# Performance work log

Hardware: AMD Instinct MI355X
Metric: run time of the kernel (lower is better)

## Reference

```python
import jax, jax.numpy as jnp
import numpy as np

K = 11            # involution kernel size
GC = 16           # involution group channels
EPS = 1e-5        # BatchNorm eps


def bn(x, g, b, m, v):
    # eval-mode BatchNorm2d with running stats
    inv = g / jnp.sqrt(v + EPS)
    return x * inv[None, :, None, None] + (b - m * inv)[None, :, None, None]


def conv1x1(x, w, b=None):
    y = jnp.einsum('bchw,oc->bohw', x, w)
    if b is not None:
        y = y + b[None, :, None, None]
    return y


def setup_inputs() -> dict:
    key = jax.random.key(0)
    ks = jax.random.split(key, 32)
    C = 128          # inplanes == planes
    Cm = C // 2      # 64, involution channels
    Mid = Cm // 4    # 16, involution reduce channels
    G = Cm // GC     # 4 groups
    SE = C // 16     # 8
    B, H, W = 1, 160, 160
    f32 = jnp.float32
    rn = lambda k, shape, s=0.05: (jax.random.normal(k, shape, dtype=f32) * s)
    pv = lambda k, n: jax.random.uniform(k, (n,), dtype=f32, minval=0.5, maxval=1.5)
    return {
        'x': jax.random.normal(ks[0], (B, C, H, W), dtype=f32),
        'g1': pv(ks[1], C), 'b1': rn(ks[2], (C,)), 'm1': rn(ks[3], (C,), 0.1), 'v1': pv(ks[4], C),
        'w1': rn(ks[5], (Cm, C)),
        'g2': pv(ks[6], Cm), 'b2': rn(ks[7], (Cm,)), 'm2': rn(ks[8], (Cm,), 0.1), 'v2': pv(ks[9], Cm),
        'inv_w1': rn(ks[10], (Mid, Cm)),
        'ig': pv(ks[11], Mid), 'ib': rn(ks[12], (Mid,)), 'im': rn(ks[13], (Mid,), 0.1), 'iv': pv(ks[14], Mid),
        'inv_w2': rn(ks[15], (K * K * G, Mid)), 'inv_b2': rn(ks[16], (K * K * G,)),
        'g3': pv(ks[17], Cm), 'b3': rn(ks[18], (Cm,)), 'm3': rn(ks[19], (Cm,), 0.1), 'v3': pv(ks[20], Cm),
        'w3': rn(ks[21], (C, Cm)),
        'se_w1': rn(ks[22], (SE, C)), 'se_b1': rn(ks[23], (SE,)),
        'se_w2': rn(ks[24], (C, SE)), 'se_b2': rn(ks[25], (C,)),
    }


def reference(x, g1, b1, m1, v1, w1, g2, b2, m2, v2,
              inv_w1, ig, ib, im, iv, inv_w2, inv_b2,
              g3, b3, m3, v3, w3, se_w1, se_b1, se_w2, se_b2):
    identity = x
    out = jax.nn.elu(bn(x, g1, b1, m1, v1))
    out = conv1x1(out, w1)                              # (B, Cm, H, W)
    out = jax.nn.elu(bn(out, g2, b2, m2, v2))

    # ----- involution(channels=Cm, kernel=11, stride=1) -----
    B, Cm, H, W = out.shape
    G = Cm // GC
    t = jax.nn.relu(bn(conv1x1(out, inv_w1), ig, ib, im, iv))
    wk = conv1x1(t, inv_w2, inv_b2)                     # (B, G*K*K, H, W)
    wk = wk.reshape(B, G, K * K, H, W)
    p = K // 2
    # patches channel order: [C, kh, kw] -> matches torch unfold
    patches = jax.lax.conv_general_dilated_patches(
        out, (K, K), (1, 1), ((p, p), (p, p)))         # (B, Cm*K*K, H, W)
    patches = patches.reshape(B, G, GC, K * K, H, W)
    out = jnp.einsum('bgkhw,bgckhw->bgchw', wk, patches).reshape(B, Cm, H, W)
    # ---------------------------------------------------------

    out = jax.nn.elu(bn(out, g3, b3, m3, v3))
    out = conv1x1(out, w3)                              # (B, C, H, W)

    # SE module
    s = out.mean(axis=(2, 3), keepdims=True)            # (B, C, 1, 1)
    s = jax.nn.relu(conv1x1(s, se_w1, se_b1))
    s = jax.nn.sigmoid(conv1x1(s, se_w2, se_b2))
    return out * s + identity
```

## Files before the change

### kernel.cpp

```cpp
#include <hip/hip_runtime.h>
#include <math.h>

#define HPIX 160
#define WPIX 160
#define NPIX 25600
#define C0   128
#define CM   64
#define MID  16
#define KK   11
#define KK2  121
#define PAD  5
#define PADW 176
#define PADH 170
#define CHP  (PADH*PADW)
#define NBX  (NPIX/256)
#define BN_EPS 1e-5f

__device__ __forceinline__ float elu_f(float y) { return y > 0.f ? y : expm1f(y); }

__global__ __launch_bounds__(256) void k_act(
        const float* __restrict__ x,
        const float* __restrict__ g1, const float* __restrict__ b1,
        const float* __restrict__ m1, const float* __restrict__ v1,
        float* __restrict__ act) {
    int i4 = blockIdx.x * 256 + threadIdx.x;
    int c = i4 / (NPIX / 4);
    float inv  = g1[c] * rsqrtf(v1[c] + BN_EPS);
    float beta = b1[c] - m1[c] * inv;
    float4 xv = ((const float4*)x)[i4];
    float4 o;
    o.x = elu_f(fmaf(xv.x, inv, beta));
    o.y = elu_f(fmaf(xv.y, inv, beta));
    o.z = elu_f(fmaf(xv.z, inv, beta));
    o.w = elu_f(fmaf(xv.w, inv, beta));
    ((float4*)act)[i4] = o;
}

__global__ __launch_bounds__(256, 4) void k_conv1(
        const float* __restrict__ act, const float* __restrict__ w1,
        const float* __restrict__ g2, const float* __restrict__ b2,
        const float* __restrict__ m2, const float* __restrict__ v2,
        float* __restrict__ feat_pad) {
    const int tid = threadIdx.x;
    const int p   = blockIdx.x * 256 + tid;
    const int oc0 = blockIdx.y * 16;
    const float* wbase = w1 + oc0 * C0;

    float acc[16] = {0,0,0,0,0,0,0,0,0,0,0,0,0,0,0,0};
    #pragma unroll 4
    for (int k = 0; k < C0; ++k) {
        float a = act[k * NPIX + p];
        #pragma unroll
        for (int j = 0; j < 16; ++j)
            acc[j] = fmaf(wbase[j * C0 + k], a, acc[j]);
    }

    const int h = p / WPIX, w = p % WPIX;
    const int off = (h + PAD) * PADW + (w + PAD);
    #pragma unroll
    for (int j = 0; j < 16; ++j) {
        int c = oc0 + j;
        float inv = g2[c] * rsqrtf(v2[c] + BN_EPS);
        float y = acc[j] * inv + (b2[c] - m2[c] * inv);
        feat_pad[c * CHP + off] = elu_f(y);
    }
}

__global__ __launch_bounds__(256, 4) void k_conv_t(
        const float* __restrict__ feat_pad, const float* __restrict__ wt,
        const float* __restrict__ g, const float* __restrict__ b,
        const float* __restrict__ m, const float* __restrict__ v,
        float* __restrict__ t) {
    const int tid = threadIdx.x;
    const int p   = blockIdx.x * 256 + tid;
    const int oc0 = blockIdx.y * 4;
    const int h = p / WPIX, w = p % WPIX;
    const int off = (h + PAD) * PADW + (w + PAD);

    float acc[4] = {0,0,0,0};
    #pragma unroll 8
    for (int k = 0; k < CM; ++k) {
        float a = feat_pad[k * CHP + off];
        #pragma unroll
        for (int j = 0; j < 4; ++j)
            acc[j] = fmaf(wt[(oc0 + j) * CM + k], a, acc[j]);
    }
    #pragma unroll
    for (int j = 0; j < 4; ++j) {
        int c = oc0 + j;
        float inv = g[c] * rsqrtf(v[c] + BN_EPS);
        t[c * NPIX + p] = fmaxf(acc[j] * inv + (b[c] - m[c] * inv), 0.f);
    }
}

__global__ __launch_bounds__(256, 4) void k_involution(
        const float* __restrict__ t, const float* __restrict__ feat_pad,
        const float* __restrict__ inv_w2, const float* __restrict__ inv_b2,
        const float* __restrict__ g3, const float* __restrict__ b3,
        const float* __restrict__ m3, const float* __restrict__ v3,
        float* __restrict__ out) {
    __shared__ float s_wk[484 * 16];
    __shared__ float s_t[MID * 16];

    const int q   = gridDim.x >> 3;
    const int b   = blockIdx.x;
    const int bid = (b & 7) * q + (b >> 3);

    const int tid = threadIdx.x;
    const int p0  = bid * 16;
    const int px  = tid & 15;
    const int c4  = tid >> 4;

    s_t[tid] = t[c4 * NPIX + p0 + px];
    __syncthreads();

    {
        float tr[MID];
        #pragma unroll
        for (int mm = 0; mm < MID; ++mm) tr[mm] = s_t[mm * 16 + px];
        for (int j = c4; j < 484; j += 16) {
            const float4* wrow = (const float4*)(inv_w2 + j * MID);
            float acc = inv_b2[j];
            #pragma unroll
            for (int qq = 0; qq < 4; ++qq) {
                float4 wv = wrow[qq];
                acc = fmaf(wv.x, tr[qq*4+0], acc);
                acc = fmaf(wv.y, tr[qq*4+1], acc);
                acc = fmaf(wv.z, tr[qq*4+2], acc);
                acc = fmaf(wv.w, tr[qq*4+3], acc);
            }
            s_wk[j * 16 + px] = acc;
        }
    }
    __syncthreads();

    const int tx = tid & 3;
    const int c  = tid >> 2;
    const int g  = c >> 4;
    const int h  = p0 / WPIX;
    const int wb = (p0 % WPIX) + tx * 4;
    const float* fbase = feat_pad + c * CHP + h * PADW + wb;
    const float* wkb   = s_wk + (g * KK2) * 16 + tx * 4;

    float acc0 = 0.f, acc1 = 0.f, acc2 = 0.f, acc3 = 0.f;
    #pragma unroll 2
    for (int kh = 0; kh < KK; ++kh) {
        const float4* fp = (const float4*)(fbase + kh * PADW);
        float4 A = fp[0], B = fp[1], Cq = fp[2], D = fp[3];
        float f[16] = {A.x,A.y,A.z,A.w, B.x,B.y,B.z,B.w,
                       Cq.x,Cq.y,Cq.z,Cq.w, D.x,D.y,D.z,D.w};
        const float* wr = wkb + kh * KK * 16;
        #pragma unroll
        for (int kw = 0; kw < KK; ++kw) {
            float4 wv = *(const float4*)(wr + kw * 16);
            acc0 = fmaf(wv.x, f[kw + 0], acc0);
            acc1 = fmaf(wv.y, f[kw + 1], acc1);
            acc2 = fmaf(wv.z, f[kw + 2], acc2);
            acc3 = fmaf(wv.w, f[kw + 3], acc3);
        }
    }

    float inv  = g3[c] * rsqrtf(v3[c] + BN_EPS);
    float beta = b3[c] - m3[c] * inv;
    float4 o;
    o.x = elu_f(fmaf(acc0, inv, beta));
    o.y = elu_f(fmaf(acc1, inv, beta));
    o.z = elu_f(fmaf(acc2, inv, beta));
    o.w = elu_f(fmaf(acc3, inv, beta));
    *(float4*)(out + c * NPIX + p0 + tx * 4) = o;
}

__global__ __launch_bounds__(256, 4) void k_conv3(
        const float* __restrict__ in, const float* __restrict__ w,
        float* __restrict__ out, float* __restrict__ parts) {
    const int tid = threadIdx.x;
    const int p   = blockIdx.x * 256 + tid;
    const int oc0 = blockIdx.y * 16;
    const float* wbase = w + oc0 * CM;

    float acc[16] = {0,0,0,0,0,0,0,0,0,0,0,0,0,0,0,0};
    #pragma unroll 4
    for (int k = 0; k < CM; ++k) {
        float a = in[k * NPIX + p];
        #pragma unroll
        for (int j = 0; j < 16; ++j)
            acc[j] = fmaf(wbase[j * CM + k], a, acc[j]);
    }
    #pragma unroll
    for (int j = 0; j < 16; ++j)
        out[(oc0 + j) * NPIX + p] = acc[j];

    __shared__ float s_red[16][4];
    const int lane = tid & 63, wid = tid >> 6;
    #pragma unroll
    for (int j = 0; j < 16; ++j) {
        float s = acc[j];
        #pragma unroll
        for (int off = 32; off; off >>= 1) s += __shfl_down(s, off);
        if (lane == 0) s_red[j][wid] = s;
    }
    __syncthreads();
    if (tid < 16) {
        float s = s_red[tid][0] + s_red[tid][1] + s_red[tid][2] + s_red[tid][3];
        parts[(oc0 + tid) * NBX + blockIdx.x] = s;
    }
}

__global__ void k_se(const float* __restrict__ parts,
                     const float* __restrict__ w1, const float* __restrict__ b1,
                     const float* __restrict__ w2, const float* __restrict__ b2,
                     float* __restrict__ scale) {
    __shared__ float s_p[C0];
    __shared__ float s_h[8];
    int tid = threadIdx.x;
    float s = 0.f;
    for (int i = 0; i < NBX; ++i) s += parts[tid * NBX + i];
    s_p[tid] = s * (1.f / NPIX);
    __syncthreads();
    if (tid < 8) {
        float acc = b1[tid];
        for (int c = 0; c < C0; ++c) acc = fmaf(w1[tid * C0 + c], s_p[c], acc);
        s_h[tid] = fmaxf(acc, 0.f);
    }
    __syncthreads();
    float acc = b2[tid];
    #pragma unroll
    for (int j = 0; j < 8; ++j) acc = fmaf(w2[tid * 8 + j], s_h[j], acc);
    scale[tid] = 1.f / (1.f + expf(-acc));
}

__global__ __launch_bounds__(256) void k_final(
        const float* __restrict__ pre, const float* __restrict__ scale,
        const float* __restrict__ x, float* __restrict__ out) {
    int i4 = blockIdx.x * 256 + threadIdx.x;
    int c = i4 / (NPIX / 4);
    float sc = scale[c];
    float4 pv = ((const float4*)pre)[i4];
    float4 xv = ((const float4*)x)[i4];
    float4 o;
    o.x = fmaf(pv.x, sc, xv.x);
    o.y = fmaf(pv.y, sc, xv.y);
    o.z = fmaf(pv.z, sc, xv.z);
    o.w = fmaf(pv.w, sc, xv.w);
    ((float4*)out)[i4] = o;
}

extern "C" void kernel_launch(void* const* d_in, const int* in_sizes, int n_in,
                              void* d_out, int out_size, void* d_ws, size_t ws_size,
                              hipStream_t stream) {
    const float* x      = (const float*)d_in[0];
    const float* g1     = (const float*)d_in[1];
    const float* b1     = (const float*)d_in[2];
    const float* m1     = (const float*)d_in[3];
    const float* v1     = (const float*)d_in[4];
    const float* w1     = (const float*)d_in[5];
    const float* g2     = (const float*)d_in[6];
    const float* b2     = (const float*)d_in[7];
    const float* m2     = (const float*)d_in[8];
    const float* v2     = (const float*)d_in[9];
    const float* inv_w1 = (const float*)d_in[10];
    const float* ig     = (const float*)d_in[11];
    const float* ib     = (const float*)d_in[12];
    const float* im     = (const float*)d_in[13];
    const float* iv     = (const float*)d_in[14];
    const float* inv_w2 = (const float*)d_in[15];
    const float* inv_b2 = (const float*)d_in[16];
    const float* g3     = (const float*)d_in[17];
    const float* b3     = (const float*)d_in[18];
    const float* m3     = (const float*)d_in[19];
    const float* v3     = (const float*)d_in[20];
    const float* w3     = (const float*)d_in[21];
    const float* se_w1  = (const float*)d_in[22];
    const float* se_b1  = (const float*)d_in[23];
    const float* se_w2  = (const float*)d_in[24];
    const float* se_b2  = (const float*)d_in[25];
    float* out = (float*)d_out;

    float* ws       = (float*)d_ws;
    float* act      = ws;
    float* feat_pad = act + C0 * NPIX;
    float* buf_t    = feat_pad + CM * CHP;
    float* buf5     = act;
    float* buf6     = buf_t + MID * NPIX;
    float* parts    = feat_pad;
    float* scale    = buf6 + C0 * NPIX;

    hipMemsetAsync(feat_pad, 0, (size_t)CM * CHP * sizeof(float), stream);

    k_act<<<(C0 * NPIX / 4) / 256, 256, 0, stream>>>(x, g1, b1, m1, v1, act);

    k_conv1<<<dim3(NBX, CM / 16), 256, 0, stream>>>(
        act, w1, g2, b2, m2, v2, feat_pad);

    k_conv_t<<<dim3(NBX, MID / 4), 256, 0, stream>>>(
        feat_pad, inv_w1, ig, ib, im, iv, buf_t);

    k_involution<<<NPIX / 16, 256, 0, stream>>>(buf_t, feat_pad, inv_w2, inv_b2,
                                                g3, b3, m3, v3, buf5);

    k_conv3<<<dim3(NBX, C0 / 16), 256, 0, stream>>>(buf5, w3, buf6, parts);

    k_se<<<1, C0, 0, stream>>>(parts, se_w1, se_b1, se_w2, se_b2, scale);

    k_final<<<(C0 * NPIX / 4) / 256, 256, 0, stream>>>(buf6, scale, x, out);
}
```

Baseline: 123.9 us.

## Halve involution block size with two channels per thread; vectorize conv weight loads

The involution kernel now runs 128 threads per block, and each thread computes two channels. This lets the same shared-memory kernel weights serve two channels' feature loads, and the dynamic-kernel generation step computes two rows per iteration with split accumulators. The 1x1 conv kernels (conv1, conv_t, conv3) now load four input channels at a time and read weights as float4 instead of scalars. The aim is fewer instructions per FMA and more reuse, at the cost of higher register pressure and fewer threads per block in the involution kernel.

Measured after the change: 148.0 us. 1.19x slower.

```diff
diff --git a/kernel.cpp b/kernel.cpp
--- a/kernel.cpp
+++ b/kernel.cpp
@@ -47,12 +47,20 @@
     const float* wbase = w1 + oc0 * C0;
 
     float acc[16] = {0,0,0,0,0,0,0,0,0,0,0,0,0,0,0,0};
-    #pragma unroll 4
-    for (int k = 0; k < C0; ++k) {
-        float a = act[k * NPIX + p];
-        #pragma unroll
-        for (int j = 0; j < 16; ++j)
-            acc[j] = fmaf(wbase[j * C0 + k], a, acc[j]);
+    #pragma unroll 2
+    for (int k0 = 0; k0 < C0; k0 += 4) {
+        float a0 = act[(k0 + 0) * NPIX + p];
+        float a1 = act[(k0 + 1) * NPIX + p];
+        float a2 = act[(k0 + 2) * NPIX + p];
+        float a3 = act[(k0 + 3) * NPIX + p];
+        #pragma unroll
+        for (int j = 0; j < 16; ++j) {
+            float4 wv = *(const float4*)(wbase + j * C0 + k0);
+            acc[j] = fmaf(wv.x, a0, acc[j]);
+            acc[j] = fmaf(wv.y, a1, acc[j]);
+            acc[j] = fmaf(wv.z, a2, acc[j]);
+            acc[j] = fmaf(wv.w, a3, acc[j]);
+        }
     }
 
     const int h = p / WPIX, w = p % WPIX;
@@ -78,12 +86,20 @@
     const int off = (h + PAD) * PADW + (w + PAD);
 
     float acc[4] = {0,0,0,0};
-    #pragma unroll 8
-    for (int k = 0; k < CM; ++k) {
-        float a = feat_pad[k * CHP + off];
-        #pragma unroll
-        for (int j = 0; j < 4; ++j)
-            acc[j] = fmaf(wt[(oc0 + j) * CM + k], a, acc[j]);
+    #pragma unroll 4
+    for (int k0 = 0; k0 < CM; k0 += 4) {
+        float a0 = feat_pad[(k0 + 0) * CHP + off];
+        float a1 = feat_pad[(k0 + 1) * CHP + off];
+        float a2 = feat_pad[(k0 + 2) * CHP + off];
+        float a3 = feat_pad[(k0 + 3) * CHP + off];
+        #pragma unroll
+        for (int j = 0; j < 4; ++j) {
+            float4 wv = *(const float4*)(wt + (oc0 + j) * CM + k0);
+            acc[j] = fmaf(wv.x, a0, acc[j]);
+            acc[j] = fmaf(wv.y, a1, acc[j]);
+            acc[j] = fmaf(wv.z, a2, acc[j]);
+            acc[j] = fmaf(wv.w, a3, acc[j]);
+        }
     }
     #pragma unroll
     for (int j = 0; j < 4; ++j) {
@@ -93,7 +109,7 @@
     }
 }
 
-__global__ __launch_bounds__(256, 4) void k_involution(
+__global__ __launch_bounds__(128, 4) void k_involution(
         const float* __restrict__ t, const float* __restrict__ feat_pad,
         const float* __restrict__ inv_w2, const float* __restrict__ inv_b2,
         const float* __restrict__ g3, const float* __restrict__ b3,
@@ -109,65 +125,124 @@
     const int tid = threadIdx.x;
     const int p0  = bid * 16;
     const int px  = tid & 15;
-    const int c4  = tid >> 4;
-
-    s_t[tid] = t[c4 * NPIX + p0 + px];
+
+    s_t[tid]       = t[(tid >> 4) * NPIX + p0 + (tid & 15)];
+    s_t[tid + 128] = t[((tid >> 4) + 8) * NPIX + p0 + (tid & 15)];
     __syncthreads();
 
     {
-        float tr[MID];
-        #pragma unroll
-        for (int mm = 0; mm < MID; ++mm) tr[mm] = s_t[mm * 16 + px];
-        for (int j = c4; j < 484; j += 16) {
-            const float4* wrow = (const float4*)(inv_w2 + j * MID);
-            float acc = inv_b2[j];
-            #pragma unroll
-            for (int qq = 0; qq < 4; ++qq) {
-                float4 wv = wrow[qq];
-                acc = fmaf(wv.x, tr[qq*4+0], acc);
-                acc = fmaf(wv.y, tr[qq*4+1], acc);
-                acc = fmaf(wv.z, tr[qq*4+2], acc);
-                acc = fmaf(wv.w, tr[qq*4+3], acc);
-            }
-            s_wk[j * 16 + px] = acc;
+        float tr0  = s_t[0*16+px],  tr1  = s_t[1*16+px];
+        float tr2  = s_t[2*16+px],  tr3  = s_t[3*16+px];
+        float tr4  = s_t[4*16+px],  tr5  = s_t[5*16+px];
+        float tr6  = s_t[6*16+px],  tr7  = s_t[7*16+px];
+        float tr8  = s_t[8*16+px],  tr9  = s_t[9*16+px];
+        float tr10 = s_t[10*16+px], tr11 = s_t[11*16+px];
+        float tr12 = s_t[12*16+px], tr13 = s_t[13*16+px];
+        float tr14 = s_t[14*16+px], tr15 = s_t[15*16+px];
+        const int jb = tid >> 4;
+
+        for (int j = jb; j + 8 < 484; j += 16) {
+            const float4* wa = (const float4*)(inv_w2 + j * MID);
+            const float4* wc = (const float4*)(inv_w2 + (j + 8) * MID);
+            float4 a0 = wa[0], a1 = wa[1], a2 = wa[2], a3 = wa[3];
+            float4 c0 = wc[0], c1 = wc[1], c2 = wc[2], c3 = wc[3];
+            float aL = inv_b2[j],     aH = 0.f;
+            float cL = inv_b2[j + 8], cH = 0.f;
+            aL = fmaf(a0.x, tr0, aL);  aL = fmaf(a0.y, tr1, aL);
+            aL = fmaf(a0.z, tr2, aL);  aL = fmaf(a0.w, tr3, aL);
+            aL = fmaf(a1.x, tr4, aL);  aL = fmaf(a1.y, tr5, aL);
+            aL = fmaf(a1.z, tr6, aL);  aL = fmaf(a1.w, tr7, aL);
+            aH = fmaf(a2.x, tr8, aH);  aH = fmaf(a2.y, tr9, aH);
+            aH = fmaf(a2.z, tr10, aH); aH = fmaf(a2.w, tr11, aH);
+            aH = fmaf(a3.x, tr12, aH); aH = fmaf(a3.y, tr13, aH);
+            aH = fmaf(a3.z, tr14, aH); aH = fmaf(a3.w, tr15, aH);
+            cL = fmaf(c0.x, tr0, cL);  cL = fmaf(c0.y, tr1, cL);
+            cL = fmaf(c0.z, tr2, cL);  cL = fmaf(c0.w, tr3, cL);
+            cL = fmaf(c1.x, tr4, cL);  cL = fmaf(c1.y, tr5, cL);
+            cL = fmaf(c1.z, tr6, cL);  cL = fmaf(c1.w, tr7, cL);
+            cH = fmaf(c2.x, tr8, cH);  cH = fmaf(c2.y, tr9, cH);
+            cH = fmaf(c2.z, tr10, cH); cH = fmaf(c2.w, tr11, cH);
+            cH = fmaf(c3.x, tr12, cH); cH = fmaf(c3.y, tr13, cH);
+            cH = fmaf(c3.z, tr14, cH); cH = fmaf(c3.w, tr15, cH);
+            s_wk[j * 16 + px]       = aL + aH;
+            s_wk[(j + 8) * 16 + px] = cL + cH;
+        }
+        if (jb < 4) {
+            int j = 480 + jb;
+            const float4* wa = (const float4*)(inv_w2 + j * MID);
+            float4 a0 = wa[0], a1 = wa[1], a2 = wa[2], a3 = wa[3];
+            float aL = inv_b2[j], aH = 0.f;
+            aL = fmaf(a0.x, tr0, aL);  aL = fmaf(a0.y, tr1, aL);
+            aL = fmaf(a0.z, tr2, aL);  aL = fmaf(a0.w, tr3, aL);
+            aL = fmaf(a1.x, tr4, aL);  aL = fmaf(a1.y, tr5, aL);
+            aL = fmaf(a1.z, tr6, aL);  aL = fmaf(a1.w, tr7, aL);
+            aH = fmaf(a2.x, tr8, aH);  aH = fmaf(a2.y, tr9, aH);
+            aH = fmaf(a2.z, tr10, aH); aH = fmaf(a2.w, tr11, aH);
+            aH = fmaf(a3.x, tr12, aH); aH = fmaf(a3.y, tr13, aH);
+            aH = fmaf(a3.z, tr14, aH); aH = fmaf(a3.w, tr15, aH);
+            s_wk[j * 16 + px] = aL + aH;
         }
     }
     __syncthreads();
 
     const int tx = tid & 3;
-    const int c  = tid >> 2;
-    const int g  = c >> 4;
+    const int cp = tid >> 2;
+    const int c0 = cp * 2;
+    const int g  = c0 >> 4;
     const int h  = p0 / WPIX;
     const int wb = (p0 % WPIX) + tx * 4;
-    const float* fbase = feat_pad + c * CHP + h * PADW + wb;
-    const float* wkb   = s_wk + (g * KK2) * 16 + tx * 4;
-
-    float acc0 = 0.f, acc1 = 0.f, acc2 = 0.f, acc3 = 0.f;
+    const float* f0b = feat_pad + c0 * CHP + h * PADW + wb;
+    const float* f1b = f0b + CHP;
+    const float* wkb = s_wk + (g * KK2) * 16 + tx * 4;
+
+    float a00 = 0.f, a01 = 0.f, a02 = 0.f, a03 = 0.f;
+    float a10 = 0.f, a11 = 0.f, a12 = 0.f, a13 = 0.f;
     #pragma unroll 2
     for (int kh = 0; kh < KK; ++kh) {
-        const float4* fp = (const float4*)(fbase + kh * PADW);
-        float4 A = fp[0], B = fp[1], Cq = fp[2], D = fp[3];
-        float f[16] = {A.x,A.y,A.z,A.w, B.x,B.y,B.z,B.w,
-                       Cq.x,Cq.y,Cq.z,Cq.w, D.x,D.y,D.z,D.w};
+        const float4* p0f = (const float4*)(f0b + kh * PADW);
+        float4 A0 = p0f[0], B0 = p0f[1], Cq0 = p0f[2], D0 = p0f[3];
+        const float4* p1f = (const float4*)(f1b + kh * PADW);
+        float4 A1 = p1f[0], B1 = p1f[1], Cq1 = p1f[2], D1 = p1f[3];
+        float f0[16] = {A0.x,A0.y,A0.z,A0.w, B0.x,B0.y,B0.z,B0.w,
+                        Cq0.x,Cq0.y,Cq0.z,Cq0.w, D0.x,D0.y,D0.z,D0.w};
+        float f1[16] = {A1.x,A1.y,A1.z,A1.w, B1.x,B1.y,B1.z,B1.w,
+                        Cq1.x,Cq1.y,Cq1.z,Cq1.w, D1.x,D1.y,D1.z,D1.w};
         const float* wr = wkb + kh * KK * 16;
         #pragma unroll
         for (int kw = 0; kw < KK; ++kw) {
             float4 wv = *(const float4*)(wr + kw * 16);
-            acc0 = fmaf(wv.x, f[kw + 0], acc0);
-            acc1 = fmaf(wv.y, f[kw + 1], acc1);
-            acc2 = fmaf(wv.z, f[kw + 2], acc2);
-            acc3 = fmaf(wv.w, f[kw + 3], acc3);
-        }
-    }
-
-    float inv  = g3[c] * rsqrtf(v3[c] + BN_EPS);
-    float beta = b3[c] - m3[c] * inv;
-    float4 o;
-    o.x = elu_f(fmaf(acc0, inv, beta));
-    o.y = elu_f(fmaf(acc1, inv, beta));
-    o.z = elu_f(fmaf(acc2, inv, beta));
-    o.w = elu_f(fmaf(acc3, inv, beta));
-    *(float4*)(out + c * NPIX + p0 + tx * 4) = o;
+            a00 = fmaf(wv.x, f0[kw + 0], a00);
+            a01 = fmaf(wv.y, f0[kw + 1], a01);
+            a02 = fmaf(wv.z, f0[kw + 2], a02);
+            a03 = fmaf(wv.w, f0[kw + 3], a03);
+            a10 = fmaf(wv.x, f1[kw + 0], a10);
+            a11 = fmaf(wv.y, f1[kw + 1], a11);
+            a12 = fmaf(wv.z, f1[kw + 2], a12);
+            a13 = fmaf(wv.w, f1[kw + 3], a13);
+        }
+    }
+
+    {
+        float inv  = g3[c0] * rsqrtf(v3[c0] + BN_EPS);
+        float beta = b3[c0] - m3[c0] * inv;
+        float4 o;
+        o.x = elu_f(fmaf(a00, inv, beta));
+        o.y = elu_f(fmaf(a01, inv, beta));
+        o.z = elu_f(fmaf(a02, inv, beta));
+        o.w = elu_f(fmaf(a03, inv, beta));
+        *(float4*)(out + c0 * NPIX + p0 + tx * 4) = o;
+    }
+    {
+        int c1 = c0 + 1;
+        float inv  = g3[c1] * rsqrtf(v3[c1] + BN_EPS);
+        float beta = b3[c1] - m3[c1] * inv;
+        float4 o;
+        o.x = elu_f(fmaf(a10, inv, beta));
+        o.y = elu_f(fmaf(a11, inv, beta));
+        o.z = elu_f(fmaf(a12, inv, beta));
+        o.w = elu_f(fmaf(a13, inv, beta));
+        *(float4*)(out + c1 * NPIX + p0 + tx * 4) = o;
+    }
 }
 
 __global__ __launch_bounds__(256, 4) void k_conv3(
@@ -179,12 +254,20 @@
     const float* wbase = w + oc0 * CM;
 
     float acc[16] = {0,0,0,0,0,0,0,0,0,0,0,0,0,0,0,0};
-    #pragma unroll 4
-    for (int k = 0; k < CM; ++k) {
-        float a = in[k * NPIX + p];
-        #pragma unroll
-        for (int j = 0; j < 16; ++j)
-            acc[j] = fmaf(wbase[j * CM + k], a, acc[j]);
+    #pragma unroll 2
+    for (int k0 = 0; k0 < CM; k0 += 4) {
+        float a0 = in[(k0 + 0) * NPIX + p];
+        float a1 = in[(k0 + 1) * NPIX + p];
+        float a2 = in[(k0 + 2) * NPIX + p];
+        float a3 = in[(k0 + 3) * NPIX + p];
+        #pragma unroll
+        for (int j = 0; j < 16; ++j) {
+            float4 wv = *(const float4*)(wbase + j * CM + k0);
+            acc[j] = fmaf(wv.x, a0, acc[j]);
+            acc[j] = fmaf(wv.y, a1, acc[j]);
+            acc[j] = fmaf(wv.z, a2, acc[j]);
+            acc[j] = fmaf(wv.w, a3, acc[j]);
+        }
     }
     #pragma unroll
     for (int j = 0; j < 16; ++j)
@@ -295,7 +378,7 @@
     k_conv_t<<<dim3(NBX, MID / 4), 256, 0, stream>>>(
         feat_pad, inv_w1, ig, ib, im, iv, buf_t);
 
-    k_involution<<<NPIX / 16, 256, 0, stream>>>(buf_t, feat_pad, inv_w2, inv_b2,
+    k_involution<<<NPIX / 16, 128, 0, stream>>>(buf_t, feat_pad, inv_w2, inv_b2,
                                                 g3, b3, m3, v3, buf5);
 
     k_conv3<<<dim3(NBX, C0 / 16), 256, 0, stream>>>(buf5, w3, buf6, parts);
```

## Halve involution block size, two channels per thread, split kernel-weight LDS in phases

Applied to the files above, without the earlier changes.

The involution kernel now runs with 128 threads per block, and each thread computes two channels so the shared kernel weights are reused across both. The generated per-pixel kernel weights are built in two phases (rows 0-4, then rows 5-10) into an LDS buffer about half the previous size, with barriers between phases. The aim is to cut LDS use per block to raise occupancy and to amortize the LDS weight reads. In exchange it adds extra synchronization and doubles the per-thread register use for feature rows.

New measurement: 128.7 us. 1.04x slower.

```diff
diff --git a/kernel.cpp b/kernel.cpp
--- a/kernel.cpp
+++ b/kernel.cpp
@@ -93,13 +93,13 @@
     }
 }
 
-__global__ __launch_bounds__(256, 4) void k_involution(
+__global__ __launch_bounds__(128, 4) void k_involution(
         const float* __restrict__ t, const float* __restrict__ feat_pad,
         const float* __restrict__ inv_w2, const float* __restrict__ inv_b2,
         const float* __restrict__ g3, const float* __restrict__ b3,
         const float* __restrict__ m3, const float* __restrict__ v3,
         float* __restrict__ out) {
-    __shared__ float s_wk[484 * 16];
+    __shared__ float s_wk[4 * 66 * 16];
     __shared__ float s_t[MID * 16];
 
     const int q   = gridDim.x >> 3;
@@ -109,65 +109,142 @@
     const int tid = threadIdx.x;
     const int p0  = bid * 16;
     const int px  = tid & 15;
-    const int c4  = tid >> 4;
-
-    s_t[tid] = t[c4 * NPIX + p0 + px];
-    __syncthreads();
-
-    {
-        float tr[MID];
-        #pragma unroll
-        for (int mm = 0; mm < MID; ++mm) tr[mm] = s_t[mm * 16 + px];
-        for (int j = c4; j < 484; j += 16) {
-            const float4* wrow = (const float4*)(inv_w2 + j * MID);
-            float acc = inv_b2[j];
-            #pragma unroll
-            for (int qq = 0; qq < 4; ++qq) {
-                float4 wv = wrow[qq];
-                acc = fmaf(wv.x, tr[qq*4+0], acc);
-                acc = fmaf(wv.y, tr[qq*4+1], acc);
-                acc = fmaf(wv.z, tr[qq*4+2], acc);
-                acc = fmaf(wv.w, tr[qq*4+3], acc);
-            }
-            s_wk[j * 16 + px] = acc;
-        }
-    }
-    __syncthreads();
+    const int jb  = tid >> 4;
+
+    s_t[tid]       = t[(tid >> 4) * NPIX + p0 + px];
+    s_t[tid + 128] = t[((tid >> 4) + 8) * NPIX + p0 + px];
+    __syncthreads();
+
+    const float tr0  = s_t[0*16+px],  tr1  = s_t[1*16+px];
+    const float tr2  = s_t[2*16+px],  tr3  = s_t[3*16+px];
+    const float tr4  = s_t[4*16+px],  tr5  = s_t[5*16+px];
+    const float tr6  = s_t[6*16+px],  tr7  = s_t[7*16+px];
+    const float tr8  = s_t[8*16+px],  tr9  = s_t[9*16+px];
+    const float tr10 = s_t[10*16+px], tr11 = s_t[11*16+px];
+    const float tr12 = s_t[12*16+px], tr13 = s_t[13*16+px];
+    const float tr14 = s_t[14*16+px], tr15 = s_t[15*16+px];
+
+#define WK_DOT(JSRC, DST) { \
+    const float4* wrow_ = (const float4*)(inv_w2 + (JSRC) * MID); \
+    float4 w0_ = wrow_[0], w1_ = wrow_[1], w2_ = wrow_[2], w3_ = wrow_[3]; \
+    float lo_ = inv_b2[JSRC], hi_ = 0.f; \
+    lo_ = fmaf(w0_.x, tr0,  lo_); lo_ = fmaf(w0_.y, tr1,  lo_); \
+    lo_ = fmaf(w0_.z, tr2,  lo_); lo_ = fmaf(w0_.w, tr3,  lo_); \
+    lo_ = fmaf(w1_.x, tr4,  lo_); lo_ = fmaf(w1_.y, tr5,  lo_); \
+    lo_ = fmaf(w1_.z, tr6,  lo_); lo_ = fmaf(w1_.w, tr7,  lo_); \
+    hi_ = fmaf(w2_.x, tr8,  hi_); hi_ = fmaf(w2_.y, tr9,  hi_); \
+    hi_ = fmaf(w2_.z, tr10, hi_); hi_ = fmaf(w2_.w, tr11, hi_); \
+    hi_ = fmaf(w3_.x, tr12, hi_); hi_ = fmaf(w3_.y, tr13, hi_); \
+    hi_ = fmaf(w3_.z, tr14, hi_); hi_ = fmaf(w3_.w, tr15, hi_); \
+    s_wk[(DST) * 16 + px] = lo_ + hi_; }
 
     const int tx = tid & 3;
-    const int c  = tid >> 2;
-    const int g  = c >> 4;
+    const int cp = tid >> 2;
+    const int c0 = cp * 2;
+    const int g  = c0 >> 4;
     const int h  = p0 / WPIX;
     const int wb = (p0 % WPIX) + tx * 4;
-    const float* fbase = feat_pad + c * CHP + h * PADW + wb;
-    const float* wkb   = s_wk + (g * KK2) * 16 + tx * 4;
-
-    float acc0 = 0.f, acc1 = 0.f, acc2 = 0.f, acc3 = 0.f;
+    const float* f0b = feat_pad + c0 * CHP + h * PADW + wb;
+    const float* f1b = f0b + CHP;
+
+    float a00 = 0.f, a01 = 0.f, a02 = 0.f, a03 = 0.f;
+    float a10 = 0.f, a11 = 0.f, a12 = 0.f, a13 = 0.f;
+
+    for (int jj = jb; jj < 220; jj += 16) {
+        int gA = jj / 55, jlA = jj - gA * 55;
+        WK_DOT(gA * 121 + jlA, jj);
+        int jj2 = jj + 8;
+        if (jj2 < 220) {
+            int gB = jj2 / 55, jlB = jj2 - gB * 55;
+            WK_DOT(gB * 121 + jlB, jj2);
+        }
+    }
+    __syncthreads();
+
     #pragma unroll 2
-    for (int kh = 0; kh < KK; ++kh) {
-        const float4* fp = (const float4*)(fbase + kh * PADW);
-        float4 A = fp[0], B = fp[1], Cq = fp[2], D = fp[3];
-        float f[16] = {A.x,A.y,A.z,A.w, B.x,B.y,B.z,B.w,
-                       Cq.x,Cq.y,Cq.z,Cq.w, D.x,D.y,D.z,D.w};
-        const float* wr = wkb + kh * KK * 16;
+    for (int kh = 0; kh < 5; ++kh) {
+        const float4* p0f = (const float4*)(f0b + kh * PADW);
+        float4 A0 = p0f[0], B0 = p0f[1], Cq0 = p0f[2], D0 = p0f[3];
+        const float4* p1f = (const float4*)(f1b + kh * PADW);
+        float4 A1 = p1f[0], B1 = p1f[1], Cq1 = p1f[2], D1 = p1f[3];
+        float f0[16] = {A0.x,A0.y,A0.z,A0.w, B0.x,B0.y,B0.z,B0.w,
+                        Cq0.x,Cq0.y,Cq0.z,Cq0.w, D0.x,D0.y,D0.z,D0.w};
+        float f1[16] = {A1.x,A1.y,A1.z,A1.w, B1.x,B1.y,B1.z,B1.w,
+                        Cq1.x,Cq1.y,Cq1.z,Cq1.w, D1.x,D1.y,D1.z,D1.w};
+        const float* wr = s_wk + (g * 55 + kh * 11) * 16 + tx * 4;
         #pragma unroll
         for (int kw = 0; kw < KK; ++kw) {
             float4 wv = *(const float4*)(wr + kw * 16);
-            acc0 = fmaf(wv.x, f[kw + 0], acc0);
-            acc1 = fmaf(wv.y, f[kw + 1], acc1);
-            acc2 = fmaf(wv.z, f[kw + 2], acc2);
-            acc3 = fmaf(wv.w, f[kw + 3], acc3);
+            a00 = fmaf(wv.x, f0[kw + 0], a00);
+            a01 = fmaf(wv.y, f0[kw + 1], a01);
+            a02 = fmaf(wv.z, f0[kw + 2], a02);
+            a03 = fmaf(wv.w, f0[kw + 3], a03);
+            a10 = fmaf(wv.x, f1[kw + 0], a10);
+            a11 = fmaf(wv.y, f1[kw + 1], a11);
+            a12 = fmaf(wv.z, f1[kw + 2], a12);
+            a13 = fmaf(wv.w, f1[kw + 3], a13);
         }
     }
-
-    float inv  = g3[c] * rsqrtf(v3[c] + BN_EPS);
-    float beta = b3[c] - m3[c] * inv;
-    float4 o;
-    o.x = elu_f(fmaf(acc0, inv, beta));
-    o.y = elu_f(fmaf(acc1, inv, beta));
-    o.z = elu_f(fmaf(acc2, inv, beta));
-    o.w = elu_f(fmaf(acc3, inv, beta));
-    *(float4*)(out + c * NPIX + p0 + tx * 4) = o;
+    __syncthreads();
+
+    for (int jj = jb; jj < 264; jj += 16) {
+        int gA = jj / 66, jlA = jj - gA * 66;
+        WK_DOT(gA * 121 + 55 + jlA, jj);
+        int jj2 = jj + 8;
+        if (jj2 < 264) {
+            int gB = jj2 / 66, jlB = jj2 - gB * 66;
+            WK_DOT(gB * 121 + 55 + jlB, jj2);
+        }
+    }
+    __syncthreads();
+
+    #pragma unroll 2
+    for (int kh = 5; kh < 11; ++kh) {
+        const float4* p0f = (const float4*)(f0b + kh * PADW);
+        float4 A0 = p0f[0], B0 = p0f[1], Cq0 = p0f[2], D0 = p0f[3];
+        const float4* p1f = (const float4*)(f1b + kh * PADW);
+        float4 A1 = p1f[0], B1 = p1f[1], Cq1 = p1f[2], D1 = p1f[3];
+        float f0[16] = {A0.x,A0.y,A0.z,A0.w, B0.x,B0.y,B0.z,B0.w,
+                        Cq0.x,Cq0.y,Cq0.z,Cq0.w, D0.x,D0.y,D0.z,D0.w};
+        float f1[16] = {A1.x,A1.y,A1.z,A1.w, B1.x,B1.y,B1.z,B1.w,
+                        Cq1.x,Cq1.y,Cq1.z,Cq1.w, D1.x,D1.y,D1.z,D1.w};
+        const float* wr = s_wk + (g * 66 + (kh - 5) * 11) * 16 + tx * 4;
+        #pragma unroll
+        for (int kw = 0; kw < KK; ++kw) {
+            float4 wv = *(const float4*)(wr + kw * 16);
+            a00 = fmaf(wv.x, f0[kw + 0], a00);
+            a01 = fmaf(wv.y, f0[kw + 1], a01);
+            a02 = fmaf(wv.z, f0[kw + 2], a02);
+            a03 = fmaf(wv.w, f0[kw + 3], a03);
+            a10 = fmaf(wv.x, f1[kw + 0], a10);
+            a11 = fmaf(wv.y, f1[kw + 1], a11);
+            a12 = fmaf(wv.z, f1[kw + 2], a12);
+            a13 = fmaf(wv.w, f1[kw + 3], a13);
+        }
+    }
+#undef WK_DOT
+
+    {
+        float inv  = g3[c0] * rsqrtf(v3[c0] + BN_EPS);
+        float beta = b3[c0] - m3[c0] * inv;
+        float4 o;
+        o.x = elu_f(fmaf(a00, inv, beta));
+        o.y = elu_f(fmaf(a01, inv, beta));
+        o.z = elu_f(fmaf(a02, inv, beta));
+        o.w = elu_f(fmaf(a03, inv, beta));
+        *(float4*)(out + c0 * NPIX + p0 + tx * 4) = o;
+    }
+    {
+        int c1 = c0 + 1;
+        float inv  = g3[c1] * rsqrtf(v3[c1] + BN_EPS);
+        float beta = b3[c1] - m3[c1] * inv;
+        float4 o;
+        o.x = elu_f(fmaf(a10, inv, beta));
+        o.y = elu_f(fmaf(a11, inv, beta));
+        o.z = elu_f(fmaf(a12, inv, beta));
+        o.w = elu_f(fmaf(a13, inv, beta));
+        *(float4*)(out + c1 * NPIX + p0 + tx * 4) = o;
+    }
 }
 
 __global__ __launch_bounds__(256, 4) void k_conv3(
@@ -295,7 +372,7 @@
     k_conv_t<<<dim3(NBX, MID / 4), 256, 0, stream>>>(
         feat_pad, inv_w1, ig, ib, im, iv, buf_t);
 
-    k_involution<<<NPIX / 16, 256, 0, stream>>>(buf_t, feat_pad, inv_w2, inv_b2,
+    k_involution<<<NPIX / 16, 128, 0, stream>>>(buf_t, feat_pad, inv_w2, inv_b2,
                                                 g3, b3, m3, v3, buf5);
 
     k_conv3<<<dim3(NBX, C0 / 16), 256, 0, stream>>>(buf5, w3, buf6, parts);
```

## Split involution kernel weights into two row halves to shrink shared memory

Applied to the files above, without the earlier changes.

The per-block generated involution weights are now computed in two phases: first for kernel rows 0-4, which are applied, then for rows 5-10 into the same smaller shared buffer. Shared memory per block drops from 484x16 to 264x16 floats, and the launch-bounds occupancy hint rises from 4 to 6 blocks per CU. The weight dot product also splits its accumulation into two chains for more ILP. The cost is two extra block-wide barriers and the loss of overlap between weight generation and the main accumulation.

New measurement: 139.3 us. 1.12x slower.

```diff
diff --git a/kernel.cpp b/kernel.cpp
--- a/kernel.cpp
+++ b/kernel.cpp
@@ -93,13 +93,13 @@
     }
 }
 
-__global__ __launch_bounds__(256, 4) void k_involution(
+__global__ __launch_bounds__(256, 6) void k_involution(
         const float* __restrict__ t, const float* __restrict__ feat_pad,
         const float* __restrict__ inv_w2, const float* __restrict__ inv_b2,
         const float* __restrict__ g3, const float* __restrict__ b3,
         const float* __restrict__ m3, const float* __restrict__ v3,
         float* __restrict__ out) {
-    __shared__ float s_wk[484 * 16];
+    __shared__ float s_wk[4 * 66 * 16];
     __shared__ float s_t[MID * 16];
 
     const int q   = gridDim.x >> 3;
@@ -109,30 +109,33 @@
     const int tid = threadIdx.x;
     const int p0  = bid * 16;
     const int px  = tid & 15;
-    const int c4  = tid >> 4;
-
-    s_t[tid] = t[c4 * NPIX + p0 + px];
-    __syncthreads();
-
-    {
-        float tr[MID];
-        #pragma unroll
-        for (int mm = 0; mm < MID; ++mm) tr[mm] = s_t[mm * 16 + px];
-        for (int j = c4; j < 484; j += 16) {
-            const float4* wrow = (const float4*)(inv_w2 + j * MID);
-            float acc = inv_b2[j];
-            #pragma unroll
-            for (int qq = 0; qq < 4; ++qq) {
-                float4 wv = wrow[qq];
-                acc = fmaf(wv.x, tr[qq*4+0], acc);
-                acc = fmaf(wv.y, tr[qq*4+1], acc);
-                acc = fmaf(wv.z, tr[qq*4+2], acc);
-                acc = fmaf(wv.w, tr[qq*4+3], acc);
-            }
-            s_wk[j * 16 + px] = acc;
-        }
-    }
-    __syncthreads();
+    const int jb  = tid >> 4;
+
+    if (tid < MID * 16) s_t[tid] = t[(tid >> 4) * NPIX + p0 + px];
+    __syncthreads();
+
+    const float tr0  = s_t[0*16+px],  tr1  = s_t[1*16+px];
+    const float tr2  = s_t[2*16+px],  tr3  = s_t[3*16+px];
+    const float tr4  = s_t[4*16+px],  tr5  = s_t[5*16+px];
+    const float tr6  = s_t[6*16+px],  tr7  = s_t[7*16+px];
+    const float tr8  = s_t[8*16+px],  tr9  = s_t[9*16+px];
+    const float tr10 = s_t[10*16+px], tr11 = s_t[11*16+px];
+    const float tr12 = s_t[12*16+px], tr13 = s_t[13*16+px];
+    const float tr14 = s_t[14*16+px], tr15 = s_t[15*16+px];
+
+#define WK_DOT(JSRC, DST) { \
+    const float4* wrow_ = (const float4*)(inv_w2 + (JSRC) * MID); \
+    float4 w0_ = wrow_[0], w1_ = wrow_[1], w2_ = wrow_[2], w3_ = wrow_[3]; \
+    float lo_ = inv_b2[JSRC], hi_ = 0.f; \
+    lo_ = fmaf(w0_.x, tr0,  lo_); lo_ = fmaf(w0_.y, tr1,  lo_); \
+    lo_ = fmaf(w0_.z, tr2,  lo_); lo_ = fmaf(w0_.w, tr3,  lo_); \
+    lo_ = fmaf(w1_.x, tr4,  lo_); lo_ = fmaf(w1_.y, tr5,  lo_); \
+    lo_ = fmaf(w1_.z, tr6,  lo_); lo_ = fmaf(w1_.w, tr7,  lo_); \
+    hi_ = fmaf(w2_.x, tr8,  hi_); hi_ = fmaf(w2_.y, tr9,  hi_); \
+    hi_ = fmaf(w2_.z, tr10, hi_); hi_ = fmaf(w2_.w, tr11, hi_); \
+    hi_ = fmaf(w3_.x, tr12, hi_); hi_ = fmaf(w3_.y, tr13, hi_); \
+    hi_ = fmaf(w3_.z, tr14, hi_); hi_ = fmaf(w3_.w, tr15, hi_); \
+    s_wk[(DST) * 16 + px] = lo_ + hi_; }
 
     const int tx = tid & 3;
     const int c  = tid >> 2;
@@ -140,16 +143,22 @@
     const int h  = p0 / WPIX;
     const int wb = (p0 % WPIX) + tx * 4;
     const float* fbase = feat_pad + c * CHP + h * PADW + wb;
-    const float* wkb   = s_wk + (g * KK2) * 16 + tx * 4;
 
     float acc0 = 0.f, acc1 = 0.f, acc2 = 0.f, acc3 = 0.f;
+
+    #pragma unroll
+    for (int gg = 0; gg < 4; ++gg)
+        for (int jl = jb; jl < 55; jl += 16)
+            WK_DOT(gg * 121 + jl, gg * 55 + jl);
+    __syncthreads();
+
     #pragma unroll 2
-    for (int kh = 0; kh < KK; ++kh) {
+    for (int kh = 0; kh < 5; ++kh) {
         const float4* fp = (const float4*)(fbase + kh * PADW);
         float4 A = fp[0], B = fp[1], Cq = fp[2], D = fp[3];
         float f[16] = {A.x,A.y,A.z,A.w, B.x,B.y,B.z,B.w,
                        Cq.x,Cq.y,Cq.z,Cq.w, D.x,D.y,D.z,D.w};
-        const float* wr = wkb + kh * KK * 16;
+        const float* wr = s_wk + (g * 55 + kh * 11) * 16 + tx * 4;
         #pragma unroll
         for (int kw = 0; kw < KK; ++kw) {
             float4 wv = *(const float4*)(wr + kw * 16);
@@ -159,6 +168,31 @@
             acc3 = fmaf(wv.w, f[kw + 3], acc3);
         }
     }
+    __syncthreads();
+
+    #pragma unroll
+    for (int gg = 0; gg < 4; ++gg)
+        for (int jl = jb; jl < 66; jl += 16)
+            WK_DOT(gg * 121 + 55 + jl, gg * 66 + jl);
+    __syncthreads();
+
+    #pragma unroll 2
+    for (int kh = 5; kh < 11; ++kh) {
+        const float4* fp = (const float4*)(fbase + kh * PADW);
+        float4 A = fp[0], B = fp[1], Cq = fp[2], D = fp[3];
+        float f[16] = {A.x,A.y,A.z,A.w, B.x,B.y,B.z,B.w,
+                       Cq.x,Cq.y,Cq.z,Cq.w, D.x,D.y,D.z,D.w};
+        const float* wr = s_wk + (g * 66 + (kh - 5) * 11) * 16 + tx * 4;
+        #pragma unroll
+        for (int kw = 0; kw < KK; ++kw) {
+            float4 wv = *(const float4*)(wr + kw * 16);
+            acc0 = fmaf(wv.x, f[kw + 0], acc0);
+            acc1 = fmaf(wv.y, f[kw + 1], acc1);
+            acc2 = fmaf(wv.z, f[kw + 2], acc2);
+            acc3 = fmaf(wv.w, f[kw + 3], acc3);
+        }
+    }
+#undef WK_DOT
 
     float inv  = g3[c] * rsqrtf(v3[c] + BN_EPS);
     float beta = b3[c] - m3[c] * inv;
```
